# Optimization experiments

Hardware: AMD Instinct MI355X
Metric: run time of the kernel (lower is better)

The kernel has to match this reference:

```python
import jax, jax.numpy as jnp
import numpy as np

NUM_HEADS = 16
EMBED = 1024
BLOCK = 2048
VOCAB = 32000
HEAD = EMBED // NUM_HEADS


def setup_inputs() -> dict:
    key = jax.random.key(0)
    ks = jax.random.split(key, 9)
    B, T = 2, 2048
    x = jax.random.randint(ks[0], (B, T), 0, VOCAB)
    target = jax.random.randint(ks[1], (B, T), 0, VOCAB)
    s = 0.02
    tok_emb = jax.random.normal(ks[2], (VOCAB, EMBED), jnp.float32) * s
    pos_emb = jax.random.normal(ks[3], (BLOCK, EMBED), jnp.float32) * s
    Wq = jax.random.normal(ks[4], (EMBED, EMBED), jnp.float32) * s
    Wk = jax.random.normal(ks[5], (EMBED, EMBED), jnp.float32) * s
    Wv = jax.random.normal(ks[6], (EMBED, EMBED), jnp.float32) * s
    W_lm = jax.random.normal(ks[7], (EMBED, VOCAB), jnp.float32) * s
    b_lm = jnp.zeros((VOCAB,), jnp.float32)
    return {"x": x, "target": target, "tok_emb": tok_emb, "pos_emb": pos_emb,
            "Wq": Wq, "Wk": Wk, "Wv": Wv, "W_lm": W_lm, "b_lm": b_lm}


def reference(x, target, tok_emb, pos_emb, Wq, Wk, Wv, W_lm, b_lm):
    B, T = x.shape
    h = tok_emb[x] + pos_emb[:T]                       # [B,T,E]
    # fused QKV projections, then split into heads (equivalent to per-head Linears + concat)
    q = (h @ Wq).reshape(B, T, NUM_HEADS, HEAD)
    k = (h @ Wk).reshape(B, T, NUM_HEADS, HEAD)
    v = (h @ Wv).reshape(B, T, NUM_HEADS, HEAD)
    scores = jnp.einsum("bqhd,bkhd->bhqk", q, k) / (HEAD ** 0.5)
    causal = jnp.tril(jnp.ones((T, T), bool))
    scores = jnp.where(causal, scores, -jnp.inf)
    attn = jax.nn.softmax(scores, axis=-1)             # [B,H,T,T]
    out = jnp.einsum("bhqk,bkhd->bqhd", attn, v).reshape(B, T, EMBED)
    logits = out @ W_lm + b_lm                         # [B,T,V]
    logits_flat = logits.reshape(B * T, VOCAB)
    logp = jax.nn.log_softmax(logits_flat, axis=-1)
    loss = -jnp.take_along_axis(logp, target.reshape(-1, 1), axis=-1).mean()
    return logits_flat, loss
```

## Files before the change

kernel.cpp:

```cpp
#include <hip/hip_runtime.h>
#include <cstdint>
#include <cstddef>

#define EMB   1024
#define TSEQ  2048
#define NBATCH 2
#define NHEAD 16
#define HDIM  64
#define VOCAB 32000
#define ROWS  4096
#define NCB   125

typedef __attribute__((ext_vector_type(8))) short short8;
typedef __attribute__((ext_vector_type(4))) float f32x4;

__device__ __forceinline__ unsigned short f2bf(float f) {
  unsigned int u = __float_as_uint(f);
  u = (u + 0x7FFFu + ((u >> 16) & 1u)) >> 16;
  return (unsigned short)u;
}

__device__ __forceinline__ void gload16(const void* g, void* l) {
  typedef __attribute__((address_space(1))) const unsigned int gu;
  typedef __attribute__((address_space(3))) unsigned int lu;
  __builtin_amdgcn_global_load_lds((gu*)g, (lu*)l, 16, 0, 0);
}

__global__ void convT(const float* __restrict__ in, unsigned short* __restrict__ out,
                      int R, int C) {
  __shared__ float tile[32][33];
  const int ct = blockIdx.x, rt = blockIdx.y;
  const int t = threadIdx.x;
  const int r0 = t >> 5;
  const int c  = t & 31;
#pragma unroll
  for (int i = 0; i < 4; ++i) {
    int r = r0 + i * 8;
    tile[r][c] = in[(size_t)(rt * 32 + r) * C + ct * 32 + c];
  }
  __syncthreads();
#pragma unroll
  for (int i = 0; i < 4; ++i) {
    int r = r0 + i * 8;
    out[(size_t)(ct * 32 + r) * R + rt * 32 + c] = f2bf(tile[c][r]);
  }
}

__global__ void embed_kernel(const int* __restrict__ x, const float* __restrict__ tok,
                             const float* __restrict__ pos, unsigned short* __restrict__ h) {
  const int idx = blockIdx.x * 256 + threadIdx.x;
  const int row = idx >> 8;
  const int c4  = idx & 255;
  const int tpos = row & (TSEQ - 1);
  const int token = x[row];
  float4 a = *(const float4*)(tok + (size_t)token * EMB + c4 * 4);
  float4 p = *(const float4*)(pos + (size_t)tpos * EMB + c4 * 4);
  unsigned int lo = (unsigned int)f2bf(a.x + p.x) | ((unsigned int)f2bf(a.y + p.y) << 16);
  unsigned int hi = (unsigned int)f2bf(a.z + p.z) | ((unsigned int)f2bf(a.w + p.w) << 16);
  *(uint2*)(h + (size_t)idx * 4) = make_uint2(lo, hi);
}

template <int EPI>
__global__ void gemm_bt(const unsigned short* __restrict__ A,
                        const unsigned short* __restrict__ Bt,
                        void* __restrict__ Cout,
                        float scale, int M, int N, int K) {
  __shared__ unsigned short As[2][128 * 32];
  __shared__ unsigned short Bs[2][128 * 32];
  const int t  = threadIdx.x;
  const int l  = t & 63;
  const int w  = t >> 6;
  const int wr = w >> 1, wc = w & 1;
  const int m0 = blockIdx.y * 128;
  const int n0 = blockIdx.x * 128;
  const int KT = K >> 5;

  f32x4 acc[4][4] = {};

  const int crow = t >> 2;
  const int coff = (t & 3) * 16;
  const size_t abase = ((size_t)(m0 + crow) * K) * 2 + coff;
  const size_t bbase = ((size_t)(n0 + crow) * K) * 2 + coff;
  const size_t rstep = (size_t)64 * K * 2;
  const char* Ab = (const char*)A;
  const char* Bb = (const char*)Bt;

#define STAGE(buf, kt_) do {                                              \
    size_t ko = (size_t)(kt_) * 64;                                       \
    gload16(Ab + abase + ko,         (char*)&As[(buf)][0] + t * 16);      \
    gload16(Ab + abase + rstep + ko, (char*)&As[(buf)][0] + t * 16 + 4096);\
    gload16(Bb + bbase + ko,         (char*)&Bs[(buf)][0] + t * 16);      \
    gload16(Bb + bbase + rstep + ko, (char*)&Bs[(buf)][0] + t * 16 + 4096);\
  } while (0)

  const int lr  = l & 15;
  const int lkb = (l >> 4) * 16;

#define COMPUTE(buf) do {                                                  \
    const char* ab = (const char*)&As[(buf)][0];                           \
    const char* bb = (const char*)&Bs[(buf)][0];                           \
    short8 fa[4], fb[4];                                                   \
    _Pragma("unroll")                                                      \
    for (int m = 0; m < 4; ++m)                                            \
      fa[m] = *(const short8*)(ab + (wr * 64 + m * 16 + lr) * 64 + lkb);   \
    _Pragma("unroll")                                                      \
    for (int n = 0; n < 4; ++n)                                            \
      fb[n] = *(const short8*)(bb + (wc * 64 + n * 16 + lr) * 64 + lkb);   \
    _Pragma("unroll")                                                      \
    for (int m = 0; m < 4; ++m)                                            \
      _Pragma("unroll")                                                    \
      for (int n = 0; n < 4; ++n)                                          \
        acc[m][n] = __builtin_amdgcn_mfma_f32_16x16x32_bf16(               \
            fa[m], fb[n], acc[m][n], 0, 0, 0);                             \
  } while (0)

  STAGE(0, 0);
  __syncthreads();
  int cur = 0;
  for (int kt = 0; kt < KT; ++kt) {
    if (kt + 1 < KT) STAGE(cur ^ 1, kt + 1);
    COMPUTE(cur);
    __syncthreads();
    cur ^= 1;
  }
#undef STAGE
#undef COMPUTE

  const int orow = m0 + wr * 64 + (l >> 4) * 4;
  const int ocol = n0 + wc * 64 + lr;
#pragma unroll
  for (int m = 0; m < 4; ++m) {
#pragma unroll
    for (int n = 0; n < 4; ++n) {
      const int col = ocol + n * 16;
      if (EPI == 1) {
        unsigned short* C = (unsigned short*)Cout;
#pragma unroll
        for (int r = 0; r < 4; ++r) {
          int row = orow + m * 16 + r;
          C[(size_t)row * N + col] = f2bf(acc[m][n][r] * scale);
        }
      } else {
        unsigned short* C = (unsigned short*)Cout;
        int row0 = orow + m * 16;
        int bb_ = row0 >> 11, tq = row0 & 2047;
        int hh = col >> 6, dd = col & 63;
        unsigned int lo = (unsigned int)f2bf(acc[m][n][0]) | ((unsigned int)f2bf(acc[m][n][1]) << 16);
        unsigned int hi = (unsigned int)f2bf(acc[m][n][2]) | ((unsigned int)f2bf(acc[m][n][3]) << 16);
        *(uint2*)&C[(((size_t)(bb_ * NHEAD + hh) * HDIM + dd) * TSEQ) + tq] = make_uint2(lo, hi);
      }
    }
  }
}

__global__ __launch_bounds__(256)
void attn_mfma(const unsigned short* __restrict__ Qbf,
               const unsigned short* __restrict__ Kbf,
               const unsigned short* __restrict__ Vtbf,
               unsigned short* __restrict__ Obf) {
  const int qt = (gridDim.x - 1) - blockIdx.x;
  const int h  = blockIdx.y;
  const int b  = blockIdx.z;
  const int t  = threadIdx.x, w = t >> 6, l = t & 63;
  const int g  = l >> 4, c = l & 15;
  const int qw = qt * 64 + w * 16;
  const int qg = qw + c;

  __shared__ unsigned short Ks[2][32 * 64];
  __shared__ unsigned short Vs[2][64 * 32];

  const unsigned short* Qrow = Qbf + ((size_t)(b * TSEQ + qg) * EMB + h * HDIM);
  short8 qfrag[2];
  qfrag[0] = *(const short8*)(Qrow + g * 8);
  qfrag[1] = *(const short8*)(Qrow + g * 8 + 32);

  f32x4 accO[4] = {};
  float mrun = -3e38f, lsum = 0.0f;

  const int kvt = t >> 3, kch = t & 7;
  const char* Kg = (const char*)(Kbf + ((size_t)(b * TSEQ + kvt) * EMB + h * HDIM))
                   + (((kch * 16) ^ ((kvt & 7) << 4)));
  const int dt = t >> 2, vch = t & 3;
  const char* Vg = (const char*)(Vtbf + (((size_t)(b * NHEAD + h) * HDIM + dt) * TSEQ))
                   + vch * 16;
  const size_t kstep = (size_t)32 * EMB * 2;
  const size_t vstep = (size_t)32 * 2;

#define ASTAGE(buf, kt_) do {                                               \
    gload16(Kg + (size_t)(kt_) * kstep, (char*)&Ks[buf][0] + t * 16);       \
    gload16(Vg + (size_t)(kt_) * vstep, (char*)&Vs[buf][0] + t * 16);       \
  } while (0)

  const int nkt = 2 * qt + 2;
  ASTAGE(0, 0);
  __syncthreads();
  int cur = 0;
  for (int kt = 0; kt < nkt; ++kt) {
    if (kt + 1 < nkt) ASTAGE(cur ^ 1, kt + 1);
    const int k0 = kt * 32;

    const char* kb = (const char*)&Ks[cur][0];
    f32x4 sa[2] = {};
#pragma unroll
    for (int kc = 0; kc < 2; ++kc) {
#pragma unroll
      for (int kh = 0; kh < 2; ++kh) {
        short8 ka = *(const short8*)(kb + (kc * 16 + c) * 128 +
                                     ((g * 16 + kh * 64) ^ ((c & 7) << 4)));
        sa[kc] = __builtin_amdgcn_mfma_f32_16x16x32_bf16(ka, qfrag[kh], sa[kc], 0, 0, 0);
      }
    }

    float sv[8];
#pragma unroll
    for (int kc = 0; kc < 2; ++kc)
#pragma unroll
      for (int r = 0; r < 4; ++r) {
        int kv = k0 + kc * 16 + g * 4 + r;
        sv[kc * 4 + r] = (kv > qg) ? -3e38f : sa[kc][r];
      }
    float pm = sv[0];
#pragma unroll
    for (int i = 1; i < 8; ++i) pm = fmaxf(pm, sv[i]);
    pm = fmaxf(pm, __shfl_xor(pm, 16));
    pm = fmaxf(pm, __shfl_xor(pm, 32));
    const float mnew = fmaxf(mrun, pm);
    const float alpha = __expf(mrun - mnew);
    float ps = 0.0f;
#pragma unroll
    for (int i = 0; i < 8; ++i) { float p = __expf(sv[i] - mnew); sv[i] = p; ps += p; }
    ps += __shfl_xor(ps, 16);
    ps += __shfl_xor(ps, 32);
    lsum = lsum * alpha + ps;
    mrun = mnew;

#pragma unroll
    for (int r = 0; r < 4; ++r) {
      float ar = __shfl(alpha, g * 4 + r);
      accO[0][r] *= ar; accO[1][r] *= ar; accO[2][r] *= ar; accO[3][r] *= ar;
    }

    unsigned int wf[4];
#pragma unroll
    for (int rp = 0; rp < 2; ++rp)
#pragma unroll
      for (int kc = 0; kc < 2; ++kc) {
        unsigned int rw;
        asm("v_cvt_pk_bf16_f32 %0, %1, %2"
            : "=v"(rw) : "v"(sv[kc * 4 + 2 * rp]), "v"(sv[kc * 4 + 2 * rp + 1]));
        wf[rp * 2 + kc] = rw;
      }

    union { unsigned int u[4]; short8 s8; } pa;
#pragma unroll
    for (int jp = 0; jp < 4; ++jp) {
      int srcLane = c + ((2 * (g & 1) + (jp >> 1)) << 4);
      unsigned int v0 = (unsigned int)__shfl((int)wf[2 * (jp & 1)], srcLane);
      unsigned int v1 = (unsigned int)__shfl((int)wf[2 * (jp & 1) + 1], srcLane);
      pa.u[jp] = (g >> 1) ? v1 : v0;
    }

    const char* vb = (const char*)&Vs[cur][0];
#pragma unroll
    for (int cp = 0; cp < 4; ++cp) {
      short8 vf = *(const short8*)(vb + (c + 16 * cp) * 64 + g * 16);
      accO[cp] = __builtin_amdgcn_mfma_f32_16x16x32_bf16(pa.s8, vf, accO[cp], 0, 0, 0);
    }

    __syncthreads();
    cur ^= 1;
  }
#undef ASTAGE

  const float inv = 1.0f / lsum;
#pragma unroll
  for (int r = 0; r < 4; ++r) {
    float ir = __shfl(inv, g * 4 + r);
    unsigned short* orow = Obf + ((size_t)(b * TSEQ + qw + g * 4 + r) * EMB + h * HDIM);
#pragma unroll
    for (int cp = 0; cp < 4; ++cp)
      orow[c + 16 * cp] = f2bf(accO[cp][r] * ir);
  }
}

__global__ __launch_bounds__(512, 2)
void gemm_lm(const unsigned short* __restrict__ A,
             const unsigned short* __restrict__ Bt,
             const float* __restrict__ bias,
             float* __restrict__ C,
             float* __restrict__ pm, float* __restrict__ ps) {
  extern __shared__ char lds[];
  const int t = threadIdx.x;
  const int w = t >> 6, l = t & 63;
  const int wm = w >> 2, wn = w & 3;
  const int fr = l & 15, kg = l >> 4;

  const int L  = blockIdx.x;
  const int Lp = (L & 7) * 250 + (L >> 3);
  const int g_ = Lp / 500;
  const int q_ = Lp % 500;
  const int ntile = q_ >> 2;
  const int mtile = g_ * 4 + (q_ & 3);

  const char* Ag = (const char*)A;
  const char* Bg = (const char*)Bt;

  const int srow = t >> 3;
  const int scl  = t & 7;
  const int scg  = scl ^ (srow & 7);
  size_t aoff0 = ((size_t)(mtile * 256 +       srow) * EMB) * 2 + scg * 16;
  size_t aoff1 = ((size_t)(mtile * 256 + 128 + srow) * EMB) * 2 + scg * 16;
  size_t boff0 = ((size_t)(ntile * 256 +       srow) * EMB) * 2 + scg * 16;
  size_t boff1 = ((size_t)(ntile * 256 + 128 + srow) * EMB) * 2 + scg * 16;

#define STG_A(buf_, kt_, ah_) do {                                          \
    char* d = lds + (buf_) * 65536 + (ah_) * 16384 + t * 16;                \
    const char* s = Ag + ((ah_) ? aoff1 : aoff0) + (size_t)(kt_) * 128;     \
    gload16(s, d); gload16(s + 131072, d + 8192);                           \
  } while (0)
#define STG_B(buf_, kt_, bh_) do {                                          \
    char* d = lds + (buf_) * 65536 + 32768 + (bh_) * 16384 + t * 16;        \
    const char* s = Bg + ((bh_) ? boff1 : boff0) + (size_t)(kt_) * 128;     \
    gload16(s, d); gload16(s + 131072, d + 8192);                           \
  } while (0)

  const int xr  = fr & 7;
  const int cb0 = (kg ^ xr) * 16;
  const int arow = (wm * 128 + fr) * 128;
  const int brow = (wn * 64 + fr) * 128;

  f32x4 acc[8][4] = {};
  short8 fa[4][2], fb[4][2];

#define MFMA_Q(MH, NH)                                                       \
  _Pragma("unroll")                                                          \
  for (int mi = 0; mi < 4; ++mi)                                             \
    _Pragma("unroll")                                                        \
    for (int ni = 0; ni < 2; ++ni)                                           \
      _Pragma("unroll")                                                      \
      for (int ks = 0; ks < 2; ++ks)                                         \
        acc[(MH)*4+mi][(NH)*2+ni] = __builtin_amdgcn_mfma_f32_16x16x32_bf16( \
            fa[mi][ks], fb[(NH)*2+ni][ks], acc[(MH)*4+mi][(NH)*2+ni], 0,0,0);

#define TILE(h_, S1, S2, VMN) do {                                           \
    const int buf_ = (h_) & 1;                                               \
    char* Abase = lds + buf_ * 65536;                                        \
    char* Bbase = Abase + 32768;                                             \
                                                            \
    _Pragma("unroll")                                                        \
    for (int mi = 0; mi < 4; ++mi) {                                         \
      fa[mi][0] = *(const short8*)(Abase + arow + mi*2048 + cb0);            \
      fa[mi][1] = *(const short8*)(Abase + arow + mi*2048 + (cb0^64));       \
    }                                                                        \
    _Pragma("unroll")                                                        \
    for (int ni = 0; ni < 2; ++ni) {                                         \
      fb[ni][0] = *(const short8*)(Bbase + brow + ni*2048 + cb0);            \
      fb[ni][1] = *(const short8*)(Bbase + brow + ni*2048 + (cb0^64));       \
    }                                                                        \
    if (S1) STG_A(buf_^1, (h_)+1, 0);                                        \
    __builtin_amdgcn_s_barrier();                                            \
    __builtin_amdgcn_s_setprio(1); MFMA_Q(0,0); __builtin_amdgcn_s_setprio(0);\
    __builtin_amdgcn_s_barrier();                                            \
                                                            \
    _Pragma("unroll")                                                        \
    for (int ni = 0; ni < 2; ++ni) {                                         \
      fb[2+ni][0] = *(const short8*)(Bbase + brow + (2+ni)*2048 + cb0);      \
      fb[2+ni][1] = *(const short8*)(Bbase + brow + (2+ni)*2048 + (cb0^64));  \
    }                                                                        \
    if (S1) STG_A(buf_^1, (h_)+1, 1);                                        \
    __builtin_amdgcn_s_barrier();                                            \
    __builtin_amdgcn_s_setprio(1); MFMA_Q(0,1); __builtin_amdgcn_s_setprio(0);\
    __builtin_amdgcn_s_barrier();                                            \
                                                            \
    _Pragma("unroll")                                                        \
    for (int mi = 0; mi < 4; ++mi) {                                         \
      fa[mi][0] = *(const short8*)(Abase + arow + (4+mi)*2048 + cb0);        \
      fa[mi][1] = *(const short8*)(Abase + arow + (4+mi)*2048 + (cb0^64));   \
    }                                                                        \
    if (S2) STG_B(buf_, (h_)+2, 0);                                          \
    __builtin_amdgcn_s_barrier();                                            \
    __builtin_amdgcn_s_setprio(1); MFMA_Q(1,1); __builtin_amdgcn_s_setprio(0);\
    __builtin_amdgcn_s_barrier();                                            \
                                                            \
    if (S2) STG_B(buf_, (h_)+2, 1);                                          \
    __builtin_amdgcn_s_barrier();                                            \
    __builtin_amdgcn_s_setprio(1); MFMA_Q(1,0); __builtin_amdgcn_s_setprio(0);\
    if (VMN) asm volatile("s_waitcnt vmcnt(4)" ::: "memory");                \
    else     asm volatile("s_waitcnt vmcnt(0)" ::: "memory");                \
    __builtin_amdgcn_s_barrier();                                            \
  } while (0)

  STG_B(0, 0, 0); STG_B(0, 0, 1); STG_A(0, 0, 0); STG_A(0, 0, 1);
  STG_B(1, 1, 0); STG_B(1, 1, 1);
  asm volatile("s_waitcnt vmcnt(4)" ::: "memory");
  __builtin_amdgcn_s_barrier();

  for (int h = 0; h < 14; ++h) TILE(h, 1, 1, 4);
  TILE(14, 1, 0, 0);
  TILE(15, 0, 0, 0);
#undef TILE
#undef MFMA_Q
#undef STG_A
#undef STG_B

  __syncthreads();

  const int mrow0 = mtile * 256 + wm * 128;
  const int ncol0 = ntile * 256 + wn * 64;
  float biasv[4];
#pragma unroll
  for (int ni = 0; ni < 4; ++ni) biasv[ni] = bias[ncol0 + ni * 16 + fr];
#pragma unroll
  for (int mi = 0; mi < 8; ++mi)
#pragma unroll
    for (int ni = 0; ni < 4; ++ni)
#pragma unroll
      for (int rr = 0; rr < 4; ++rr)
        acc[mi][ni][rr] += biasv[ni];

#pragma unroll
  for (int mi = 0; mi < 8; ++mi)
#pragma unroll
    for (int rr = 0; rr < 4; ++rr) {
      int row = mrow0 + mi * 16 + kg * 4 + rr;
      float* cr = C + (size_t)row * VOCAB + ncol0 + fr;
#pragma unroll
      for (int ni = 0; ni < 4; ++ni) cr[ni * 16] = acc[mi][ni][rr];
    }

  float* redm = (float*)lds;
  float* reds = (float*)(lds + 4096);
#pragma unroll
  for (int mi = 0; mi < 8; ++mi)
#pragma unroll
    for (int rr = 0; rr < 4; ++rr) {
      float m1 = fmaxf(fmaxf(acc[mi][0][rr], acc[mi][1][rr]),
                       fmaxf(acc[mi][2][rr], acc[mi][3][rr]));
      m1 = fmaxf(m1, __shfl_xor(m1, 1));
      m1 = fmaxf(m1, __shfl_xor(m1, 2));
      m1 = fmaxf(m1, __shfl_xor(m1, 4));
      m1 = fmaxf(m1, __shfl_xor(m1, 8));
      if (fr == 0) redm[(wm * 4 + wn) * 128 + mi * 16 + kg * 4 + rr] = m1;
    }
  __syncthreads();

  float rmx[8][4];
#pragma unroll
  for (int mi = 0; mi < 8; ++mi)
#pragma unroll
    for (int rr = 0; rr < 4; ++rr) {
      int row = mi * 16 + kg * 4 + rr;
      float a0 = fmaxf(redm[(wm*4+0)*128 + row], redm[(wm*4+1)*128 + row]);
      float a1 = fmaxf(redm[(wm*4+2)*128 + row], redm[(wm*4+3)*128 + row]);
      rmx[mi][rr] = fmaxf(a0, a1);
    }
#pragma unroll
  for (int mi = 0; mi < 8; ++mi)
#pragma unroll
    for (int rr = 0; rr < 4; ++rr) {
      float r = rmx[mi][rr];
      float s1 = __expf(acc[mi][0][rr] - r) + __expf(acc[mi][1][rr] - r)
               + __expf(acc[mi][2][rr] - r) + __expf(acc[mi][3][rr] - r);
      s1 += __shfl_xor(s1, 1);
      s1 += __shfl_xor(s1, 2);
      s1 += __shfl_xor(s1, 4);
      s1 += __shfl_xor(s1, 8);
      if (fr == 0) reds[(wm * 4 + wn) * 128 + mi * 16 + kg * 4 + rr] = s1;
    }
  __syncthreads();

  if (wn == 0 && fr == 0) {
#pragma unroll
    for (int mi = 0; mi < 8; ++mi)
#pragma unroll
      for (int rr = 0; rr < 4; ++rr) {
        int row = mi * 16 + kg * 4 + rr;
        float ssum = reds[(wm*4+0)*128 + row] + reds[(wm*4+1)*128 + row]
                   + reds[(wm*4+2)*128 + row] + reds[(wm*4+3)*128 + row];
        int grow = mrow0 + row;
        pm[(size_t)grow * NCB + ntile] = rmx[mi][rr];
        ps[(size_t)grow * NCB + ntile] = ssum;
      }
  }
}

__global__ void loss_rows2(const float* __restrict__ pm, const float* __restrict__ ps,
                           const float* __restrict__ logits, const int* __restrict__ tgt,
                           float* __restrict__ partial) {
  const int row = blockIdx.x * 4 + (threadIdx.x >> 6);
  const int l = threadIdx.x & 63;
  const float* pmr = pm + (size_t)row * NCB;
  const float* psr = ps + (size_t)row * NCB;
  float m = -3e38f, s = 0.0f;
  for (int i = l; i < NCB; i += 64) {
    float mv = pmr[i], sv = psr[i];
    float nm = fmaxf(m, mv);
    s = s * __expf(m - nm) + sv * __expf(mv - nm);
    m = nm;
  }
#pragma unroll
  for (int off = 1; off < 64; off <<= 1) {
    float om = __shfl_xor(m, off), os = __shfl_xor(s, off);
    float nm = fmaxf(m, om);
    s = s * __expf(m - nm) + os * __expf(om - nm);
    m = nm;
  }
  if (l == 0) {
    float lse = m + __logf(s);
    partial[row] = -(logits[(size_t)row * VOCAB + tgt[row]] - lse);
  }
}

__global__ void loss_final(const float* __restrict__ partial, float* __restrict__ out) {
  const int t = threadIdx.x;
  float s = 0.0f;
  for (int i = t; i < ROWS; i += 256) s += partial[i];
#pragma unroll
  for (int off = 1; off < 64; off <<= 1) s += __shfl_xor(s, off);
  __shared__ float ws_[4];
  if ((t & 63) == 0) ws_[t >> 6] = s;
  __syncthreads();
  if (t == 0) out[0] = (ws_[0] + ws_[1] + ws_[2] + ws_[3]) * (1.0f / (float)ROWS);
}

extern "C" void kernel_launch(void* const* d_in, const int* in_sizes, int n_in,
                              void* d_out, int out_size, void* d_ws, size_t ws_size,
                              hipStream_t stream) {
  const int*   x      = (const int*)d_in[0];
  const int*   target = (const int*)d_in[1];
  const float* tok    = (const float*)d_in[2];
  const float* pos    = (const float*)d_in[3];
  const float* Wq     = (const float*)d_in[4];
  const float* Wk     = (const float*)d_in[5];
  const float* Wv     = (const float*)d_in[6];
  const float* Wlm    = (const float*)d_in[7];
  const float* blm    = (const float*)d_in[8];
  float* out = (float*)d_out;

  char* p = (char*)d_ws;
  unsigned short* Wqt  = (unsigned short*)p; p += (size_t)EMB * EMB * 2;
  unsigned short* Wkt  = (unsigned short*)p; p += (size_t)EMB * EMB * 2;
  unsigned short* Wvt  = (unsigned short*)p; p += (size_t)EMB * EMB * 2;
  unsigned short* Wlmt = (unsigned short*)p; p += (size_t)VOCAB * EMB * 2;
  unsigned short* hbf  = (unsigned short*)p; p += (size_t)ROWS * EMB * 2;
  unsigned short* qbf  = (unsigned short*)p; p += (size_t)ROWS * EMB * 2;
  unsigned short* kbf  = (unsigned short*)p; p += (size_t)ROWS * EMB * 2;
  unsigned short* vtbf = (unsigned short*)p; p += (size_t)ROWS * EMB * 2;
  unsigned short* obf  = (unsigned short*)p; p += (size_t)ROWS * EMB * 2;
  float*          prt  = (float*)p;          p += (size_t)ROWS * 4;
  float*          pmw  = (float*)p;          p += (size_t)ROWS * NCB * 4;
  float*          psw  = (float*)p;          p += (size_t)ROWS * NCB * 4;

  (void)hipFuncSetAttribute((const void*)gemm_lm,
                            hipFuncAttributeMaxDynamicSharedMemorySize, 131072);

  dim3 b256(256);
  convT<<<dim3(EMB / 32, EMB / 32), b256, 0, stream>>>(Wq, Wqt, EMB, EMB);
  convT<<<dim3(EMB / 32, EMB / 32), b256, 0, stream>>>(Wk, Wkt, EMB, EMB);
  convT<<<dim3(EMB / 32, EMB / 32), b256, 0, stream>>>(Wv, Wvt, EMB, EMB);
  convT<<<dim3(VOCAB / 32, EMB / 32), b256, 0, stream>>>(Wlm, Wlmt, EMB, VOCAB);

  embed_kernel<<<ROWS * (EMB / 4) / 256, b256, 0, stream>>>(x, tok, pos, hbf);

  gemm_bt<1><<<dim3(EMB / 128, ROWS / 128), b256, 0, stream>>>(hbf, Wqt, qbf, 0.125f, ROWS, EMB, EMB);
  gemm_bt<1><<<dim3(EMB / 128, ROWS / 128), b256, 0, stream>>>(hbf, Wkt, kbf, 1.0f, ROWS, EMB, EMB);
  gemm_bt<2><<<dim3(EMB / 128, ROWS / 128), b256, 0, stream>>>(hbf, Wvt, vtbf, 1.0f, ROWS, EMB, EMB);

  attn_mfma<<<dim3(TSEQ / 64, NHEAD, NBATCH), b256, 0, stream>>>(qbf, kbf, vtbf, obf);

  gemm_lm<<<dim3((ROWS / 256) * (VOCAB / 256)), dim3(512), 131072, stream>>>(
      obf, Wlmt, blm, out, pmw, psw);

  loss_rows2<<<ROWS / 4, b256, 0, stream>>>(pmw, psw, out, target, prt);
  loss_final<<<1, b256, 0, stream>>>(prt, out + (size_t)ROWS * VOCAB);
}
```

Measured before the change: 673.7 us.

## Fuse QKV projections into one GEMM and widen attention KV tiles to 64

```diff
diff --git a/kernel.cpp b/kernel.cpp
--- a/kernel.cpp
+++ b/kernel.cpp
@@ -60,13 +60,14 @@
   *(uint2*)(h + (size_t)idx * 4) = make_uint2(lo, hi);
 }
 
-template <int EPI>
-__global__ void gemm_bt(const unsigned short* __restrict__ A,
-                        const unsigned short* __restrict__ Bt,
-                        void* __restrict__ Cout,
-                        float scale, int M, int N, int K) {
+__global__ void gemm_qkv(const unsigned short* __restrict__ A,
+                         const unsigned short* __restrict__ Bt,
+                         unsigned short* __restrict__ Qo,
+                         unsigned short* __restrict__ Ko,
+                         unsigned short* __restrict__ Vto) {
   __shared__ unsigned short As[2][128 * 32];
   __shared__ unsigned short Bs[2][128 * 32];
+  const int K = EMB;
   const int t  = threadIdx.x;
   const int l  = t & 63;
   const int w  = t >> 6;
@@ -126,6 +127,7 @@
 #undef STAGE
 #undef COMPUTE
 
+  const int sec = n0 >> 10;
   const int orow = m0 + wr * 64 + (l >> 4) * 4;
   const int ocol = n0 + wc * 64 + lr;
 #pragma unroll
@@ -133,21 +135,22 @@
 #pragma unroll
     for (int n = 0; n < 4; ++n) {
       const int col = ocol + n * 16;
-      if (EPI == 1) {
-        unsigned short* C = (unsigned short*)Cout;
-#pragma unroll
-        for (int r = 0; r < 4; ++r) {
-          int row = orow + m * 16 + r;
-          C[(size_t)row * N + col] = f2bf(acc[m][n][r] * scale);
-        }
+      const int c10 = col & 1023;
+      if (sec == 0) {
+#pragma unroll
+        for (int r = 0; r < 4; ++r)
+          Qo[(size_t)(orow + m * 16 + r) * EMB + c10] = f2bf(acc[m][n][r] * 0.125f);
+      } else if (sec == 1) {
+#pragma unroll
+        for (int r = 0; r < 4; ++r)
+          Ko[(size_t)(orow + m * 16 + r) * EMB + c10] = f2bf(acc[m][n][r]);
       } else {
-        unsigned short* C = (unsigned short*)Cout;
         int row0 = orow + m * 16;
         int bb_ = row0 >> 11, tq = row0 & 2047;
-        int hh = col >> 6, dd = col & 63;
+        int hh = c10 >> 6, dd = c10 & 63;
         unsigned int lo = (unsigned int)f2bf(acc[m][n][0]) | ((unsigned int)f2bf(acc[m][n][1]) << 16);
         unsigned int hi = (unsigned int)f2bf(acc[m][n][2]) | ((unsigned int)f2bf(acc[m][n][3]) << 16);
-        *(uint2*)&C[(((size_t)(bb_ * NHEAD + hh) * HDIM + dd) * TSEQ) + tq] = make_uint2(lo, hi);
+        *(uint2*)&Vto[(((size_t)(bb_ * NHEAD + hh) * HDIM + dd) * TSEQ) + tq] = make_uint2(lo, hi);
       }
     }
   }
@@ -166,8 +169,8 @@
   const int qw = qt * 64 + w * 16;
   const int qg = qw + c;
 
-  __shared__ unsigned short Ks[2][32 * 64];
-  __shared__ unsigned short Vs[2][64 * 32];
+  __shared__ unsigned short Ks[2][64 * 64];
+  __shared__ unsigned short Vs[2][64 * 64];
 
   const unsigned short* Qrow = Qbf + ((size_t)(b * TSEQ + qg) * EMB + h * HDIM);
   short8 qfrag[2];
@@ -177,94 +180,108 @@
   f32x4 accO[4] = {};
   float mrun = -3e38f, lsum = 0.0f;
 
-  const int kvt = t >> 3, kch = t & 7;
-  const char* Kg = (const char*)(Kbf + ((size_t)(b * TSEQ + kvt) * EMB + h * HDIM))
-                   + (((kch * 16) ^ ((kvt & 7) << 4)));
-  const int dt = t >> 2, vch = t & 3;
-  const char* Vg = (const char*)(Vtbf + (((size_t)(b * NHEAD + h) * HDIM + dt) * TSEQ))
-                   + vch * 16;
-  const size_t kstep = (size_t)32 * EMB * 2;
-  const size_t vstep = (size_t)32 * 2;
-
-#define ASTAGE(buf, kt_) do {                                               \
-    gload16(Kg + (size_t)(kt_) * kstep, (char*)&Ks[buf][0] + t * 16);       \
-    gload16(Vg + (size_t)(kt_) * vstep, (char*)&Vs[buf][0] + t * 16);       \
+  const int srw = t >> 2, sch = t & 3;
+  const char* Kg = (const char*)(Kbf + ((size_t)(b * TSEQ + srw) * EMB + h * HDIM))
+                   + ((sch ^ (srw & 7)) * 16);
+  const char* Vg = (const char*)(Vtbf + (((size_t)(b * NHEAD + h) * HDIM + srw) * TSEQ))
+                   + ((sch ^ (srw & 7)) * 16);
+  const size_t kstep = (size_t)64 * EMB * 2;
+  const size_t vstep = (size_t)64 * 2;
+  const int sdst = srw * 128 + sch * 16;
+
+#define ASTAGE(buf, n_) do {                                                \
+    const char* ks = Kg + (size_t)(n_) * kstep;                             \
+    char* kd = (char*)&Ks[buf][0] + sdst;                                   \
+    gload16(ks, kd);                                                        \
+    gload16((const char*)((uintptr_t)ks ^ 64), kd + 64);                    \
+    const char* vs = Vg + (size_t)(n_) * vstep;                             \
+    char* vd = (char*)&Vs[buf][0] + sdst;                                   \
+    gload16(vs, vd);                                                        \
+    gload16((const char*)((uintptr_t)vs ^ 64), vd + 64);                    \
   } while (0)
 
-  const int nkt = 2 * qt + 2;
+  const int nkt = qt + 1;
   ASTAGE(0, 0);
   __syncthreads();
   int cur = 0;
-  for (int kt = 0; kt < nkt; ++kt) {
-    if (kt + 1 < nkt) ASTAGE(cur ^ 1, kt + 1);
-    const int k0 = kt * 32;
+  for (int n = 0; n < nkt; ++n) {
+    if (n + 1 < nkt) ASTAGE(cur ^ 1, n + 1);
+    const int k0 = n * 64;
 
     const char* kb = (const char*)&Ks[cur][0];
-    f32x4 sa[2] = {};
-#pragma unroll
-    for (int kc = 0; kc < 2; ++kc) {
-#pragma unroll
-      for (int kh = 0; kh < 2; ++kh) {
-        short8 ka = *(const short8*)(kb + (kc * 16 + c) * 128 +
-                                     ((g * 16 + kh * 64) ^ ((c & 7) << 4)));
-        sa[kc] = __builtin_amdgcn_mfma_f32_16x16x32_bf16(ka, qfrag[kh], sa[kc], 0, 0, 0);
+    f32x4 sa[4];
+#pragma unroll
+    for (int hh = 0; hh < 2; ++hh)
+#pragma unroll
+      for (int kc = 0; kc < 2; ++kc) {
+        f32x4 a0 = {};
+#pragma unroll
+        for (int kh = 0; kh < 2; ++kh) {
+          short8 ka = *(const short8*)(kb + (hh * 32 + kc * 16 + c) * 128 +
+                                       ((g * 16 + kh * 64) ^ ((c & 7) << 4)));
+          a0 = __builtin_amdgcn_mfma_f32_16x16x32_bf16(ka, qfrag[kh], a0, 0, 0, 0);
+        }
+        sa[hh * 2 + kc] = a0;
       }
-    }
-
-    float sv[8];
-#pragma unroll
-    for (int kc = 0; kc < 2; ++kc)
-#pragma unroll
-      for (int r = 0; r < 4; ++r) {
-        int kv = k0 + kc * 16 + g * 4 + r;
-        sv[kc * 4 + r] = (kv > qg) ? -3e38f : sa[kc][r];
-      }
-    float pm = sv[0];
-#pragma unroll
-    for (int i = 1; i < 8; ++i) pm = fmaxf(pm, sv[i]);
-    pm = fmaxf(pm, __shfl_xor(pm, 16));
-    pm = fmaxf(pm, __shfl_xor(pm, 32));
-    const float mnew = fmaxf(mrun, pm);
+
+    float sv[16];
+#pragma unroll
+    for (int hh = 0; hh < 2; ++hh)
+#pragma unroll
+      for (int kc = 0; kc < 2; ++kc)
+#pragma unroll
+        for (int r = 0; r < 4; ++r) {
+          int kv = k0 + hh * 32 + kc * 16 + g * 4 + r;
+          sv[hh * 8 + kc * 4 + r] = (kv > qg) ? -3e38f : sa[hh * 2 + kc][r];
+        }
+    float pmax = sv[0];
+#pragma unroll
+    for (int i = 1; i < 16; ++i) pmax = fmaxf(pmax, sv[i]);
+    pmax = fmaxf(pmax, __shfl_xor(pmax, 16));
+    pmax = fmaxf(pmax, __shfl_xor(pmax, 32));
+    const float mnew = fmaxf(mrun, pmax);
     const float alpha = __expf(mrun - mnew);
     float ps = 0.0f;
 #pragma unroll
-    for (int i = 0; i < 8; ++i) { float p = __expf(sv[i] - mnew); sv[i] = p; ps += p; }
+    for (int i = 0; i < 16; ++i) { float p = __expf(sv[i] - mnew); sv[i] = p; ps += p; }
     ps += __shfl_xor(ps, 16);
     ps += __shfl_xor(ps, 32);
     lsum = lsum * alpha + ps;
     mrun = mnew;
-
 #pragma unroll
     for (int r = 0; r < 4; ++r) {
       float ar = __shfl(alpha, g * 4 + r);
       accO[0][r] *= ar; accO[1][r] *= ar; accO[2][r] *= ar; accO[3][r] *= ar;
     }
 
-    unsigned int wf[4];
-#pragma unroll
-    for (int rp = 0; rp < 2; ++rp)
-#pragma unroll
-      for (int kc = 0; kc < 2; ++kc) {
-        unsigned int rw;
-        asm("v_cvt_pk_bf16_f32 %0, %1, %2"
-            : "=v"(rw) : "v"(sv[kc * 4 + 2 * rp]), "v"(sv[kc * 4 + 2 * rp + 1]));
-        wf[rp * 2 + kc] = rw;
+    const char* vb = (const char*)&Vs[cur][0];
+#pragma unroll
+    for (int hh = 0; hh < 2; ++hh) {
+      unsigned int wf[4];
+#pragma unroll
+      for (int rp = 0; rp < 2; ++rp)
+#pragma unroll
+        for (int kc = 0; kc < 2; ++kc) {
+          unsigned int rw;
+          asm("v_cvt_pk_bf16_f32 %0, %1, %2"
+              : "=v"(rw) : "v"(sv[hh * 8 + kc * 4 + 2 * rp]),
+                           "v"(sv[hh * 8 + kc * 4 + 2 * rp + 1]));
+          wf[rp * 2 + kc] = rw;
+        }
+      union { unsigned int u[4]; short8 s8; } pa;
+#pragma unroll
+      for (int jp = 0; jp < 4; ++jp) {
+        int srcLane = c + ((2 * (g & 1) + (jp >> 1)) << 4);
+        unsigned int v0 = (unsigned int)__shfl((int)wf[2 * (jp & 1)], srcLane);
+        unsigned int v1 = (unsigned int)__shfl((int)wf[2 * (jp & 1) + 1], srcLane);
+        pa.u[jp] = (g >> 1) ? v1 : v0;
       }
-
-    union { unsigned int u[4]; short8 s8; } pa;
-#pragma unroll
-    for (int jp = 0; jp < 4; ++jp) {
-      int srcLane = c + ((2 * (g & 1) + (jp >> 1)) << 4);
-      unsigned int v0 = (unsigned int)__shfl((int)wf[2 * (jp & 1)], srcLane);
-      unsigned int v1 = (unsigned int)__shfl((int)wf[2 * (jp & 1) + 1], srcLane);
-      pa.u[jp] = (g >> 1) ? v1 : v0;
-    }
-
-    const char* vb = (const char*)&Vs[cur][0];
-#pragma unroll
-    for (int cp = 0; cp < 4; ++cp) {
-      short8 vf = *(const short8*)(vb + (c + 16 * cp) * 64 + g * 16);
-      accO[cp] = __builtin_amdgcn_mfma_f32_16x16x32_bf16(pa.s8, vf, accO[cp], 0, 0, 0);
+#pragma unroll
+      for (int cp = 0; cp < 4; ++cp) {
+        short8 vf = *(const short8*)(vb + (c + 16 * cp) * 128 +
+                                     ((hh * 64 + g * 16) ^ ((c & 7) << 4)));
+        accO[cp] = __builtin_amdgcn_mfma_f32_16x16x32_bf16(pa.s8, vf, accO[cp], 0, 0, 0);
+      }
     }
 
     __syncthreads();
@@ -562,9 +579,7 @@
 
   embed_kernel<<<ROWS * (EMB / 4) / 256, b256, 0, stream>>>(x, tok, pos, hbf);
 
-  gemm_bt<1><<<dim3(EMB / 128, ROWS / 128), b256, 0, stream>>>(hbf, Wqt, qbf, 0.125f, ROWS, EMB, EMB);
-  gemm_bt<1><<<dim3(EMB / 128, ROWS / 128), b256, 0, stream>>>(hbf, Wkt, kbf, 1.0f, ROWS, EMB, EMB);
-  gemm_bt<2><<<dim3(EMB / 128, ROWS / 128), b256, 0, stream>>>(hbf, Wvt, vtbf, 1.0f, ROWS, EMB, EMB);
+  gemm_qkv<<<dim3(3 * EMB / 128, ROWS / 128), b256, 0, stream>>>(hbf, Wqt, qbf, kbf, vtbf);
 
   attn_mfma<<<dim3(TSEQ / 64, NHEAD, NBATCH), b256, 0, stream>>>(qbf, kbf, vtbf, obf);
 
```

Result: faster. 600.0 us (-10.9%).
